# Performance work log

Hardware: AMD Instinct MI355X
Metric: run time of the kernel (lower is better)

Reference implementation:

```python
import jax, jax.numpy as jnp
import numpy as np

B, S, D_IN, D_MODEL = 8, 2048, 512, 512
NEG_INF = -1e9  # matches masked_fill value -1000000000.0


def setup_inputs() -> dict:
    key = jax.random.key(0)
    ks = jax.random.split(key, 7)
    scale = 1.0 / np.sqrt(D_IN).astype(np.float32)
    return {
        "x": jax.random.normal(ks[0], (B, S, D_IN), dtype=jnp.float32),
        "pad_mask": jnp.zeros((B, S), dtype=bool),
        "Wq": jax.random.normal(ks[1], (D_MODEL, D_IN), dtype=jnp.float32) * scale,
        "bq": jax.random.normal(ks[2], (D_MODEL,), dtype=jnp.float32) * 0.01,
        "Wk": jax.random.normal(ks[3], (D_MODEL, D_IN), dtype=jnp.float32) * scale,
        "bk": jax.random.normal(ks[4], (D_MODEL,), dtype=jnp.float32) * 0.01,
        "Wv": jax.random.normal(ks[5], (D_MODEL, D_IN), dtype=jnp.float32) * scale,
        "bv": jax.random.normal(ks[6], (D_MODEL,), dtype=jnp.float32) * 0.01,
    }


def reference(x, pad_mask, Wq, bq, Wk, bk, Wv, bv):
    # Linear projections (torch Linear: y = x @ W.T + b)
    q = jnp.einsum('bsd,md->bsm', x, Wq) + bq  # [B,S,M]
    k = jnp.einsum('bsd,md->bsm', x, Wk) + bk
    v = jnp.einsum('bsd,md->bsm', x, Wv) + bv
    inv_sqrt_m = jnp.float32(1.0 / np.sqrt(D_MODEL))
    s = jnp.einsum('bqm,bkm->bqk', q, k) * inv_sqrt_m  # [B,S,S]
    # pad mask broadcasts over query dim (pad_mask.unsqueeze(1) in torch)
    s = jnp.where(pad_mask[:, None, :], NEG_INF, s)
    # masked (causal) attention: upper triangle above diagonal is blocked
    causal = jnp.triu(jnp.ones((S, S), dtype=bool), k=1)
    s = jnp.where(causal[None, :, :], NEG_INF, s)
    scores = jax.nn.softmax(s, axis=-1)
    # dropout p=0.0 / eval mode -> identity
    return jnp.einsum('bqk,bkm->bqm', scores, v)
```

## Files before the change

### kernel.cpp

```cpp
#include <hip/hip_runtime.h>
#include <hip/hip_bf16.h>


typedef __attribute__((ext_vector_type(8))) short short8;
typedef __attribute__((ext_vector_type(4))) float f32x4;

#define S_    2048
#define DM    512
#define SCALE 0.04419417382415922f

static __device__ __forceinline__ unsigned short f2bf(float f) {
    __hip_bfloat16 h = __float2bfloat16(f);
    unsigned short u;
    __builtin_memcpy(&u, &h, sizeof(u));
    return u;
}
static __device__ __forceinline__ float bf2f(unsigned short u) {
    union { unsigned int i; float f; } c;
    c.i = ((unsigned int)u) << 16;
    return c.f;
}

static __device__ __forceinline__ void gload16(const void* g, void* l) {
    __builtin_amdgcn_global_load_lds(
        (const __attribute__((address_space(1))) void*)g,
        (__attribute__((address_space(3))) void*)l, 16, 0, 0);
}

static __device__ __forceinline__ void stage_tile(
    const unsigned short* __restrict__ gbase, size_t ld,
    unsigned short (*lds)[64], int w, int lane)
{
    const int srow = lane >> 3;
    const int scol = (lane & 7) * 8;
    #pragma unroll
    for (int t = 0; t < 4; t++) {
        const int row = w * 32 + t * 8 + srow;
        gload16(gbase + (size_t)row * ld + scol, &lds[w * 32 + t * 8][0]);
    }
}

static __device__ __forceinline__ void mfma_step(
    const unsigned short (*Ash)[64], const unsigned short (*Bsh)[64],
    f32x4 acc[4][4], int wm, int wn, int lr, int lg)
{
    #pragma unroll
    for (int kk = 0; kk < 2; kk++) {
        short8 af[4], bf[4];
        #pragma unroll
        for (int m = 0; m < 4; m++)
            af[m] = *reinterpret_cast<const short8*>(&Ash[wm * 64 + m * 16 + lr][kk * 32 + lg * 8]);
        #pragma unroll
        for (int n = 0; n < 4; n++)
            bf[n] = *reinterpret_cast<const short8*>(&Bsh[wn * 64 + n * 16 + lr][kk * 32 + lg * 8]);
        #pragma unroll
        for (int m = 0; m < 4; m++)
            #pragma unroll
            for (int n = 0; n < 4; n++)
                acc[m][n] = __builtin_amdgcn_mfma_f32_16x16x32_bf16(af[m], bf[n], acc[m][n], 0, 0, 0);
    }
}

__global__ __launch_bounds__(256) void cvt_all(
    const float* __restrict__ x,
    const float* __restrict__ wq, const float* __restrict__ wk, const float* __restrict__ wv,
    unsigned short* __restrict__ xb,
    unsigned short* __restrict__ wqb, unsigned short* __restrict__ wkb,
    unsigned short* __restrict__ wvb)
{
    const int bid = blockIdx.x;
    const float* src; unsigned short* dst; int i;
    if (bid < 8192) { src = x; dst = xb; i = bid * 256 + threadIdx.x; }
    else {
        const int r = bid - 8192;
        const int m = r >> 8;
        src = (m == 0) ? wq : (m == 1) ? wk : wv;
        dst = (m == 0) ? wqb : (m == 1) ? wkb : wvb;
        i = (r & 255) * 256 + threadIdx.x;
    }
    float4 v = reinterpret_cast<const float4*>(src)[i];
    ushort4 o;
    o.x = f2bf(v.x); o.y = f2bf(v.y); o.z = f2bf(v.z); o.w = f2bf(v.w);
    reinterpret_cast<ushort4*>(dst)[i] = o;
}

__global__ __launch_bounds__(256) void qkv_gemm(
    const unsigned short* __restrict__ X,
    const unsigned short* __restrict__ W0, const unsigned short* __restrict__ W1,
    const unsigned short* __restrict__ W2,
    const float* __restrict__ b0, const float* __restrict__ b1, const float* __restrict__ b2,
    unsigned short* __restrict__ Dq, unsigned short* __restrict__ Dk,
    unsigned short* __restrict__ Dvt)
{
    __shared__ unsigned short smem[2][2][128][64];

    const int z = blockIdx.z;
    const unsigned short* __restrict__ Wb = (z == 0) ? W0 : (z == 1) ? W1 : W2;
    const float* __restrict__ bias        = (z == 0) ? b0 : (z == 1) ? b1 : b2;
    unsigned short* __restrict__ D        = (z == 0) ? Dq : (z == 1) ? Dk : Dvt;
    const bool vpath = (z == 2);
    const int m0 = vpath ? blockIdx.y * 128 : blockIdx.x * 128;
    const int n0 = vpath ? blockIdx.x * 128 : blockIdx.y * 128;
    const size_t ldD = vpath ? 16384 : 512;
    const unsigned short* __restrict__ Aop = vpath ? Wb : X;
    const unsigned short* __restrict__ Bop = vpath ? X  : Wb;

    const int tid  = threadIdx.x;
    const int lane = tid & 63;
    const int w    = tid >> 6;
    const int wm   = w >> 1, wn = w & 1;
    const int lr   = lane & 15, lg = lane >> 4;

    f32x4 acc[4][4];
    #pragma unroll
    for (int m = 0; m < 4; m++)
        #pragma unroll
        for (int n = 0; n < 4; n++) acc[m][n] = (f32x4){0.f, 0.f, 0.f, 0.f};

    stage_tile(&Aop[(size_t)m0 * DM], DM, smem[0][0], w, lane);
    stage_tile(&Bop[(size_t)n0 * DM], DM, smem[0][1], w, lane);
    __syncthreads();
    int cur = 0;
    for (int t = 0; t < 8; t++) {
        if (t < 7) {
            const int k0 = (t + 1) * 64;
            stage_tile(&Aop[(size_t)m0 * DM + k0], DM, smem[cur ^ 1][0], w, lane);
            stage_tile(&Bop[(size_t)n0 * DM + k0], DM, smem[cur ^ 1][1], w, lane);
        }
        mfma_step(smem[cur][0], smem[cur][1], acc, wm, wn, lr, lg);
        __syncthreads();
        cur ^= 1;
    }

    unsigned short (*Csh)[128] = reinterpret_cast<unsigned short (*)[128]>(&smem[0][0][0][0]);
    #pragma unroll
    for (int n = 0; n < 4; n++) {
        int ct = wn * 64 + n * 16 + lr;
        float bcol = vpath ? 0.f : bias[n0 + ct];
        #pragma unroll
        for (int m = 0; m < 4; m++) {
            int rt = wm * 64 + m * 16 + lg * 4;
            #pragma unroll
            for (int j = 0; j < 4; j++) {
                int row = rt + j;
                float bv = vpath ? bias[m0 + row] : bcol;
                Csh[row][ct ^ ((row & 7) << 3)] = f2bf(acc[m][n][j] + bv);
            }
        }
    }
    __syncthreads();
    #pragma unroll
    for (int i = 0; i < 8; i++) {
        int chunk = i * 256 + tid;
        int row = chunk >> 4, cb = (chunk & 15) * 8;
        short8 vv = *reinterpret_cast<const short8*>(&Csh[row][cb ^ ((row & 7) << 3)]);
        *reinterpret_cast<short8*>(&D[(size_t)(m0 + row) * ldD + n0 + cb]) = vv;
    }
}

__global__ __launch_bounds__(256) void qk_gemm(
    const unsigned short* __restrict__ Qg, const unsigned short* __restrict__ Kg,
    const unsigned char* __restrict__ pad, unsigned short* __restrict__ Sp,
    float* __restrict__ partial)
{
    __shared__ unsigned short smem[2][2][128][64];

    const int wgid = blockIdx.x;
    const int b = wgid & 7;
    const int l = wgid >> 3;
    int it = (int)((sqrtf(8.f * l + 1.f) - 1.f) * 0.5f);
    while ((it + 1) * (it + 2) / 2 <= l) ++it;
    while (it * (it + 1) / 2 > l) --it;
    const int jt = l - it * (it + 1) / 2;

    const unsigned short* __restrict__ A = Qg + (size_t)b * S_ * DM;
    const unsigned short* __restrict__ B = Kg + (size_t)b * S_ * DM;
    unsigned short* __restrict__ Sw = Sp + ((size_t)b * 136 + l) * 16384;
    const int m0 = it * 128, n0 = jt * 128;

    const int tid  = threadIdx.x;
    const int lane = tid & 63;
    const int w    = tid >> 6;
    const int wm   = w >> 1, wn = w & 1;
    const int lr   = lane & 15, lg = lane >> 4;

    f32x4 acc[4][4];
    #pragma unroll
    for (int m = 0; m < 4; m++)
        #pragma unroll
        for (int n = 0; n < 4; n++) acc[m][n] = (f32x4){0.f, 0.f, 0.f, 0.f};

    stage_tile(&A[(size_t)m0 * DM], DM, smem[0][0], w, lane);
    stage_tile(&B[(size_t)n0 * DM], DM, smem[0][1], w, lane);
    __syncthreads();
    int cur = 0;
    for (int t = 0; t < 8; t++) {
        if (t < 7) {
            const int k0 = (t + 1) * 64;
            stage_tile(&A[(size_t)m0 * DM + k0], DM, smem[cur ^ 1][0], w, lane);
            stage_tile(&B[(size_t)n0 * DM + k0], DM, smem[cur ^ 1][1], w, lane);
        }
        mfma_step(smem[cur][0], smem[cur][1], acc, wm, wn, lr, lg);
        __syncthreads();
        cur ^= 1;
    }

    unsigned short (*Csh)[128] = reinterpret_cast<unsigned short (*)[128]>(&smem[0][0][0][0]);
    #pragma unroll
    for (int n = 0; n < 4; n++) {
        int ct = wn * 64 + n * 16 + lr;
        int colg = n0 + ct;
        bool pd = pad[(size_t)b * S_ + colg] != 0;
        #pragma unroll
        for (int m = 0; m < 4; m++) {
            int rt = wm * 64 + m * 16 + lg * 4;
            #pragma unroll
            for (int j = 0; j < 4; j++) {
                int row = rt + j;
                float p = (pd || colg > m0 + row) ? 0.f : __expf(acc[m][n][j] * SCALE);
                Csh[row][ct ^ ((row & 7) << 3)] = f2bf(p);
            }
        }
    }
    __syncthreads();
    #pragma unroll
    for (int i = 0; i < 8; i++) {
        int chunk = i * 256 + tid;
        int row = chunk >> 4, cb = (chunk & 15) * 8;
        short8 vv = *reinterpret_cast<const short8*>(&Csh[row][cb ^ ((row & 7) << 3)]);
        *reinterpret_cast<short8*>(&Sw[(size_t)row * 128 + cb]) = vv;
        float s = 0.f;
        #pragma unroll
        for (int e = 0; e < 8; e++) s += bf2f((unsigned short)vv[e]);
        #pragma unroll
        for (int msk = 1; msk < 16; msk <<= 1) s += __shfl_xor(s, msk);
        if ((lane & 15) == 0)
            partial[((size_t)b * S_ + m0 + row) * 16 + jt] = s;
    }
}

__global__ __launch_bounds__(256) void pv_gemm(
    const unsigned short* __restrict__ Sp, const unsigned short* __restrict__ VT,
    const float* __restrict__ partial, float* __restrict__ Out)
{
    __shared__ unsigned short smem[2][2][128][64];

    const int wgid = blockIdx.x;
    const int b  = wgid & 7;
    const int r  = wgid >> 3;
    const int it = 15 - (r >> 2);
    const int nb = r & 3;
    const int m0 = it * 128, n0 = nb * 128;
    const int nt = (it + 1) * 2;
    const unsigned short* __restrict__ Abase =
        Sp + ((size_t)b * 136 + (size_t)it * (it + 1) / 2) * 16384;

    const int tid  = threadIdx.x;
    const int lane = tid & 63;
    const int w    = tid >> 6;
    const int wm   = w >> 1, wn = w & 1;
    const int lr   = lane & 15, lg = lane >> 4;

    f32x4 acc[4][4];
    #pragma unroll
    for (int m = 0; m < 4; m++)
        #pragma unroll
        for (int n = 0; n < 4; n++) acc[m][n] = (f32x4){0.f, 0.f, 0.f, 0.f};

    stage_tile(Abase, 128, smem[0][0], w, lane);
    stage_tile(&VT[(size_t)n0 * 16384 + (size_t)b * S_], 16384, smem[0][1], w, lane);
    __syncthreads();
    int cur = 0;
    for (int t = 0; t < nt; t++) {
        if (t + 1 < nt) {
            const int k0 = (t + 1) * 64;
            stage_tile(Abase + (size_t)(k0 >> 7) * 16384 + (k0 & 127), 128, smem[cur ^ 1][0], w, lane);
            stage_tile(&VT[(size_t)n0 * 16384 + (size_t)b * S_ + k0], 16384, smem[cur ^ 1][1], w, lane);
        }
        mfma_step(smem[cur][0], smem[cur][1], acc, wm, wn, lr, lg);
        __syncthreads();
        cur ^= 1;
    }

    float* Lsh = reinterpret_cast<float*>(&smem[0][0][0][0]);
    if (tid < 128) {
        const float* pr = &partial[((size_t)b * S_ + m0 + tid) * 16];
        float s = 0.f;
        for (int j = 0; j <= it; j++) s += pr[j];
        Lsh[tid] = 1.f / s;
    }
    __syncthreads();

    #pragma unroll
    for (int n = 0; n < 4; n++) {
        int col = n0 + wn * 64 + n * 16 + lr;
        #pragma unroll
        for (int m = 0; m < 4; m++) {
            int rowb = wm * 64 + m * 16 + lg * 4;
            #pragma unroll
            for (int j = 0; j < 4; j++) {
                int row = rowb + j;
                float li = Lsh[row];
                Out[((size_t)(b * S_ + m0 + row)) * DM + col] = acc[m][n][j] * li;
            }
        }
    }
}

extern "C" void kernel_launch(void* const* d_in, const int* in_sizes, int n_in,
                              void* d_out, int out_size, void* d_ws, size_t ws_size,
                              hipStream_t stream) {
    const float* x  = (const float*)d_in[0];
    const unsigned char* pad = (const unsigned char*)d_in[1];
    const float* Wq = (const float*)d_in[2];
    const float* bq = (const float*)d_in[3];
    const float* Wk = (const float*)d_in[4];
    const float* bk = (const float*)d_in[5];
    const float* Wv = (const float*)d_in[6];
    const float* bv = (const float*)d_in[7];
    float* out = (float*)d_out;

    char* ws = (char*)d_ws;
    unsigned short* vtb     = (unsigned short*)(ws);
    float*          partial = (float*)(ws + 16777216);
    unsigned short* Spacked = (unsigned short*)(ws + 17825792);
    unsigned short* xb      = (unsigned short*)(ws + 17825792);
    unsigned short* wqb     = (unsigned short*)(ws + 53477376);
    unsigned short* wkb     = wqb + 262144;
    unsigned short* wvb     = wqb + 524288;

    unsigned short* qb = (unsigned short*)d_out;
    unsigned short* kb = qb + 8388608;

    cvt_all<<<8960, 256, 0, stream>>>(x, Wq, Wk, Wv, xb, wqb, wkb, wvb);

    dim3 gq(128, 4, 3);
    qkv_gemm<<<gq, 256, 0, stream>>>(xb, wqb, wkb, wvb, bq, bk, bv, qb, kb, vtb);

    qk_gemm<<<1088, 256, 0, stream>>>(qb, kb, pad, Spacked, partial);

    pv_gemm<<<512, 256, 0, stream>>>(Spacked, vtb, partial, out);
}
```

Baseline: 131.8 us.

## Fuse Q and K projections sharing X tile; reorder pv_gemm tile schedule

The single QKV GEMM launch is split into a fused Q/K projection kernel and a separate V-transpose GEMM. The Q/K kernel loads each X tile once and feeds two accumulator sets, which halves X traffic for those projections, at the cost of more registers and a smaller K-step of 32. The pv_gemm block-to-tile mapping also changes so the second half of blocks walks the row tiles in ascending order instead of descending, interleaving long and short causal rows. The risks are an extra kernel launch and lower occupancy from 32 accumulator vectors per thread.

Result: faster. 126.4 us (median of 2 runs) (-4.1%).

```diff
diff --git a/kernel.cpp b/kernel.cpp
--- a/kernel.cpp
+++ b/kernel.cpp
@@ -37,6 +37,19 @@
     for (int t = 0; t < 4; t++) {
         const int row = w * 32 + t * 8 + srow;
         gload16(gbase + (size_t)row * ld + scol, &lds[w * 32 + t * 8][0]);
+    }
+}
+
+static __device__ __forceinline__ void stage32(
+    const unsigned short* __restrict__ gbase, size_t ld,
+    unsigned short (*lds)[32], int w, int lane)
+{
+    const int srow = lane >> 2;
+    const int scol = (lane & 3) * 8;
+    #pragma unroll
+    for (int t = 0; t < 2; t++) {
+        const int row = w * 32 + t * 16 + srow;
+        gload16(gbase + (size_t)row * ld + scol, &lds[w * 32 + t * 16][0]);
     }
 }
 
@@ -84,26 +97,16 @@
     reinterpret_cast<ushort4*>(dst)[i] = o;
 }
 
-__global__ __launch_bounds__(256) void qkv_gemm(
+__global__ __launch_bounds__(256) void qk_proj(
     const unsigned short* __restrict__ X,
-    const unsigned short* __restrict__ W0, const unsigned short* __restrict__ W1,
-    const unsigned short* __restrict__ W2,
-    const float* __restrict__ b0, const float* __restrict__ b1, const float* __restrict__ b2,
-    unsigned short* __restrict__ Dq, unsigned short* __restrict__ Dk,
-    unsigned short* __restrict__ Dvt)
-{
-    __shared__ unsigned short smem[2][2][128][64];
-
-    const int z = blockIdx.z;
-    const unsigned short* __restrict__ Wb = (z == 0) ? W0 : (z == 1) ? W1 : W2;
-    const float* __restrict__ bias        = (z == 0) ? b0 : (z == 1) ? b1 : b2;
-    unsigned short* __restrict__ D        = (z == 0) ? Dq : (z == 1) ? Dk : Dvt;
-    const bool vpath = (z == 2);
-    const int m0 = vpath ? blockIdx.y * 128 : blockIdx.x * 128;
-    const int n0 = vpath ? blockIdx.x * 128 : blockIdx.y * 128;
-    const size_t ldD = vpath ? 16384 : 512;
-    const unsigned short* __restrict__ Aop = vpath ? Wb : X;
-    const unsigned short* __restrict__ Bop = vpath ? X  : Wb;
+    const unsigned short* __restrict__ Wqb, const unsigned short* __restrict__ Wkb,
+    const float* __restrict__ bq, const float* __restrict__ bk,
+    unsigned short* __restrict__ Dq, unsigned short* __restrict__ Dk)
+{
+    __shared__ unsigned short smem[2][3][128][32];
+
+    const int m0 = blockIdx.x * 128;
+    const int n0 = blockIdx.y * 128;
 
     const int tid  = threadIdx.x;
     const int lane = tid & 63;
@@ -111,21 +114,125 @@
     const int wm   = w >> 1, wn = w & 1;
     const int lr   = lane & 15, lg = lane >> 4;
 
+    f32x4 accq[4][4], acck[4][4];
+    #pragma unroll
+    for (int m = 0; m < 4; m++)
+        #pragma unroll
+        for (int n = 0; n < 4; n++) {
+            accq[m][n] = (f32x4){0.f, 0.f, 0.f, 0.f};
+            acck[m][n] = (f32x4){0.f, 0.f, 0.f, 0.f};
+        }
+
+    stage32(&X[(size_t)m0 * DM], DM, smem[0][0], w, lane);
+    stage32(&Wqb[(size_t)n0 * DM], DM, smem[0][1], w, lane);
+    stage32(&Wkb[(size_t)n0 * DM], DM, smem[0][2], w, lane);
+    __syncthreads();
+    int cur = 0;
+    for (int t = 0; t < 16; t++) {
+        if (t < 15) {
+            const int k0 = (t + 1) * 32;
+            stage32(&X[(size_t)m0 * DM + k0], DM, smem[cur ^ 1][0], w, lane);
+            stage32(&Wqb[(size_t)n0 * DM + k0], DM, smem[cur ^ 1][1], w, lane);
+            stage32(&Wkb[(size_t)n0 * DM + k0], DM, smem[cur ^ 1][2], w, lane);
+        }
+        short8 af[4], bqf[4], bkf[4];
+        #pragma unroll
+        for (int m = 0; m < 4; m++)
+            af[m] = *reinterpret_cast<const short8*>(&smem[cur][0][wm * 64 + m * 16 + lr][lg * 8]);
+        #pragma unroll
+        for (int n = 0; n < 4; n++) {
+            bqf[n] = *reinterpret_cast<const short8*>(&smem[cur][1][wn * 64 + n * 16 + lr][lg * 8]);
+            bkf[n] = *reinterpret_cast<const short8*>(&smem[cur][2][wn * 64 + n * 16 + lr][lg * 8]);
+        }
+        #pragma unroll
+        for (int m = 0; m < 4; m++)
+            #pragma unroll
+            for (int n = 0; n < 4; n++) {
+                accq[m][n] = __builtin_amdgcn_mfma_f32_16x16x32_bf16(af[m], bqf[n], accq[m][n], 0, 0, 0);
+                acck[m][n] = __builtin_amdgcn_mfma_f32_16x16x32_bf16(af[m], bkf[n], acck[m][n], 0, 0, 0);
+            }
+        __syncthreads();
+        cur ^= 1;
+    }
+
+    unsigned short (*Csh)[128] = reinterpret_cast<unsigned short (*)[128]>(&smem[0][0][0][0]);
+    #pragma unroll
+    for (int n = 0; n < 4; n++) {
+        int ct = wn * 64 + n * 16 + lr;
+        float bcol = bq[n0 + ct];
+        #pragma unroll
+        for (int m = 0; m < 4; m++) {
+            int rt = wm * 64 + m * 16 + lg * 4;
+            #pragma unroll
+            for (int j = 0; j < 4; j++) {
+                int row = rt + j;
+                Csh[row][ct ^ ((row & 7) << 3)] = f2bf(accq[m][n][j] + bcol);
+            }
+        }
+    }
+    __syncthreads();
+    #pragma unroll
+    for (int i = 0; i < 8; i++) {
+        int chunk = i * 256 + tid;
+        int row = chunk >> 4, cb = (chunk & 15) * 8;
+        short8 vv = *reinterpret_cast<const short8*>(&Csh[row][cb ^ ((row & 7) << 3)]);
+        *reinterpret_cast<short8*>(&Dq[(size_t)(m0 + row) * DM + n0 + cb]) = vv;
+    }
+    __syncthreads();
+    #pragma unroll
+    for (int n = 0; n < 4; n++) {
+        int ct = wn * 64 + n * 16 + lr;
+        float bcol = bk[n0 + ct];
+        #pragma unroll
+        for (int m = 0; m < 4; m++) {
+            int rt = wm * 64 + m * 16 + lg * 4;
+            #pragma unroll
+            for (int j = 0; j < 4; j++) {
+                int row = rt + j;
+                Csh[row][ct ^ ((row & 7) << 3)] = f2bf(acck[m][n][j] + bcol);
+            }
+        }
+    }
+    __syncthreads();
+    #pragma unroll
+    for (int i = 0; i < 8; i++) {
+        int chunk = i * 256 + tid;
+        int row = chunk >> 4, cb = (chunk & 15) * 8;
+        short8 vv = *reinterpret_cast<const short8*>(&Csh[row][cb ^ ((row & 7) << 3)]);
+        *reinterpret_cast<short8*>(&Dk[(size_t)(m0 + row) * DM + n0 + cb]) = vv;
+    }
+}
+
+__global__ __launch_bounds__(256) void vt_gemm(
+    const unsigned short* __restrict__ X, const unsigned short* __restrict__ Wvb,
+    const float* __restrict__ bv, unsigned short* __restrict__ Dvt)
+{
+    __shared__ unsigned short smem[2][2][128][64];
+
+    const int m0 = blockIdx.y * 128;
+    const int n0 = blockIdx.x * 128;
+
+    const int tid  = threadIdx.x;
+    const int lane = tid & 63;
+    const int w    = tid >> 6;
+    const int wm   = w >> 1, wn = w & 1;
+    const int lr   = lane & 15, lg = lane >> 4;
+
     f32x4 acc[4][4];
     #pragma unroll
     for (int m = 0; m < 4; m++)
         #pragma unroll
         for (int n = 0; n < 4; n++) acc[m][n] = (f32x4){0.f, 0.f, 0.f, 0.f};
 
-    stage_tile(&Aop[(size_t)m0 * DM], DM, smem[0][0], w, lane);
-    stage_tile(&Bop[(size_t)n0 * DM], DM, smem[0][1], w, lane);
+    stage_tile(&Wvb[(size_t)m0 * DM], DM, smem[0][0], w, lane);
+    stage_tile(&X[(size_t)n0 * DM], DM, smem[0][1], w, lane);
     __syncthreads();
     int cur = 0;
     for (int t = 0; t < 8; t++) {
         if (t < 7) {
             const int k0 = (t + 1) * 64;
-            stage_tile(&Aop[(size_t)m0 * DM + k0], DM, smem[cur ^ 1][0], w, lane);
-            stage_tile(&Bop[(size_t)n0 * DM + k0], DM, smem[cur ^ 1][1], w, lane);
+            stage_tile(&Wvb[(size_t)m0 * DM + k0], DM, smem[cur ^ 1][0], w, lane);
+            stage_tile(&X[(size_t)n0 * DM + k0], DM, smem[cur ^ 1][1], w, lane);
         }
         mfma_step(smem[cur][0], smem[cur][1], acc, wm, wn, lr, lg);
         __syncthreads();
@@ -136,15 +243,13 @@
     #pragma unroll
     for (int n = 0; n < 4; n++) {
         int ct = wn * 64 + n * 16 + lr;
-        float bcol = vpath ? 0.f : bias[n0 + ct];
         #pragma unroll
         for (int m = 0; m < 4; m++) {
             int rt = wm * 64 + m * 16 + lg * 4;
             #pragma unroll
             for (int j = 0; j < 4; j++) {
                 int row = rt + j;
-                float bv = vpath ? bias[m0 + row] : bcol;
-                Csh[row][ct ^ ((row & 7) << 3)] = f2bf(acc[m][n][j] + bv);
+                Csh[row][ct ^ ((row & 7) << 3)] = f2bf(acc[m][n][j] + bv[m0 + row]);
             }
         }
     }
@@ -154,7 +259,7 @@
         int chunk = i * 256 + tid;
         int row = chunk >> 4, cb = (chunk & 15) * 8;
         short8 vv = *reinterpret_cast<const short8*>(&Csh[row][cb ^ ((row & 7) << 3)]);
-        *reinterpret_cast<short8*>(&D[(size_t)(m0 + row) * ldD + n0 + cb]) = vv;
+        *reinterpret_cast<short8*>(&Dvt[(size_t)(m0 + row) * 16384 + n0 + cb]) = vv;
     }
 }
 
@@ -248,7 +353,7 @@
     const int wgid = blockIdx.x;
     const int b  = wgid & 7;
     const int r  = wgid >> 3;
-    const int it = 15 - (r >> 2);
+    const int it = (r < 32) ? (15 - (r >> 2)) : ((r >> 2) - 8);
     const int nb = r & 3;
     const int m0 = it * 128, n0 = nb * 128;
     const int nt = (it + 1) * 2;
@@ -334,8 +439,11 @@
 
     cvt_all<<<8960, 256, 0, stream>>>(x, Wq, Wk, Wv, xb, wqb, wkb, wvb);
 
-    dim3 gq(128, 4, 3);
-    qkv_gemm<<<gq, 256, 0, stream>>>(xb, wqb, wkb, wvb, bq, bk, bv, qb, kb, vtb);
+    dim3 gp2(128, 4);
+    qk_proj<<<gp2, 256, 0, stream>>>(xb, wqb, wkb, bq, bk, qb, kb);
+
+    dim3 gv(128, 4);
+    vt_gemm<<<gv, 256, 0, stream>>>(xb, wvb, bv, vtb);
 
     qk_gemm<<<1088, 256, 0, stream>>>(qb, kb, pad, Spacked, partial);
 
```
